# Kernel tuning notes

Measured on AMD Instinct MI355X. Metric: run time of the kernel, lower is better.

Reference implementation:

```python
import jax, jax.numpy as jnp
import numpy as np

N_NODES = 100000
N_EDGES = 1600000
N_FEAT = 128
HIDDEN = 64
NUM_GRAPHS = 64


def setup_inputs() -> dict:
    key = jax.random.key(0)
    ks = jax.random.split(key, 10)
    x = jax.random.normal(ks[0], (N_NODES, N_FEAT), dtype=jnp.float32)
    W = jax.random.normal(ks[1], (N_FEAT, HIDDEN), dtype=jnp.float32) * (1.0 / np.sqrt(N_FEAT))
    b = jax.random.normal(ks[2], (HIDDEN,), dtype=jnp.float32) * 0.01
    W1 = jax.random.normal(ks[3], (HIDDEN, 16), dtype=jnp.float32) * (1.0 / np.sqrt(HIDDEN))
    b1 = jax.random.normal(ks[4], (16,), dtype=jnp.float32) * 0.01
    W2 = jax.random.normal(ks[5], (16, 1), dtype=jnp.float32) * 0.25
    b2 = jax.random.normal(ks[6], (1,), dtype=jnp.float32) * 0.01
    edge_index = jax.random.randint(ks[7], (2, N_EDGES), 0, N_NODES, dtype=jnp.int64)
    batch = jnp.sort(jax.random.randint(ks[8], (N_NODES,), 0, NUM_GRAPHS, dtype=jnp.int64))
    return {"x": x, "W": W, "b": b, "W1": W1, "b1": b1, "W2": W2, "b2": b2,
            "edge_index": edge_index, "batch": batch, "num_graphs": NUM_GRAPHS}


def reference(x, W, b, W1, b1, W2, b2, edge_index, batch, num_graphs):
    N = x.shape[0]
    # GCNConv: h = D^-1/2 (A + I) D^-1/2 (x W) + b
    h = x @ W  # [N, H]
    loops = jnp.arange(N, dtype=edge_index.dtype)
    src = jnp.concatenate([edge_index[0], loops])  # source nodes (with self-loops)
    dst = jnp.concatenate([edge_index[1], loops])  # target nodes
    deg = jax.ops.segment_sum(jnp.ones(dst.shape, h.dtype), dst, num_segments=N)
    dis = jnp.where(deg > 0, jax.lax.rsqrt(deg), 0.0)  # deg^-1/2, 0 for isolated
    norm = dis[src] * dis[dst]  # [E+N]
    msg = h[src] * norm[:, None]  # gather + normalize
    agg = jax.ops.segment_sum(msg, dst, num_segments=N) + b  # scatter-add + bias
    hn = jax.nn.relu(agg)
    # global_add_pool over graphs
    u = jax.ops.segment_sum(hn, batch, num_segments=num_graphs)  # [G, H]
    out = jax.nn.relu(u @ W1 + b1) @ W2 + b2  # [G, 1]
    return out.reshape(-1)
```

## Files before the change

### kernel.cpp

```cpp
#include <hip/hip_runtime.h>

#define N_NODES   100000
#define N_FEAT    128
#define N_EDGES   1600000
#define HIDDEN    64
#define NUM_GRAPHS 64
#define CHUNK   8192
#define NCHUNK  ((N_EDGES + CHUNK - 1) / CHUNK)
#define BSHIFT  8
#define NBUCKET ((N_NODES + 255) >> 8)
#define OFFS_W  (NBUCKET + 1)
#define CAP     4800

typedef unsigned int  uint32;
typedef unsigned short ushort16;

typedef __attribute__((ext_vector_type(8))) __bf16 bf16x8;
typedef __attribute__((ext_vector_type(4))) float  f32x4;
union Frag8 { bf16x8 v; unsigned short s[8]; uint4 q; };

static __device__ __forceinline__ unsigned short f2bf(float f) {
    uint32 u = __float_as_uint(f);
    u += 0x7fffu + ((u >> 16) & 1u);
    return (unsigned short)(u >> 16);
}

__global__ __launch_bounds__(256) void w_transpose(const float* __restrict__ W,
                                                   ushort16* __restrict__ Wt) {
    const int base = blockIdx.x * 1024 + threadIdx.x;
#pragma unroll
    for (int j = 0; j < 4; ++j) {
        const int idx = base + j * 256;
        const int k = idx >> 6, n = idx & 63;
        Wt[n * N_FEAT + k] = f2bf(W[idx]);
    }
}

__global__ __launch_bounds__(256) void gemm_xw(const float* __restrict__ x,
                                               const ushort16* __restrict__ Wt,
                                               ushort16* __restrict__ hb) {
    const int lane = threadIdx.x & 63;
    const int wv   = threadIdx.x >> 6;
    const int m15  = lane & 15;
    const int quad = lane >> 4;
    const int base = blockIdx.x * 64 + wv * 16;
    const int arow = min(base + m15, N_NODES - 1);

    const float* xr = &x[(size_t)arow * N_FEAT + quad * 8];
    float4 xa[4][2];
#pragma unroll
    for (int kc = 0; kc < 4; ++kc) {
        xa[kc][0] = *(const float4*)&xr[kc * 32];
        xa[kc][1] = *(const float4*)&xr[kc * 32 + 4];
    }

    Frag8 bf[4][4];
#pragma unroll
    for (int nt = 0; nt < 4; ++nt) {
        const ushort16* wr = &Wt[(nt * 16 + m15) * N_FEAT + quad * 8];
#pragma unroll
        for (int kc = 0; kc < 4; ++kc)
            bf[nt][kc].q = *(const uint4*)&wr[kc * 32];
    }

    Frag8 af[4];
#pragma unroll
    for (int kc = 0; kc < 4; ++kc) {
        const float* f = (const float*)&xa[kc][0];
#pragma unroll
        for (int j = 0; j < 8; ++j) af[kc].s[j] = f2bf(f[j]);
    }

    f32x4 acc[4];
#pragma unroll
    for (int nt = 0; nt < 4; ++nt) acc[nt] = (f32x4){0.f, 0.f, 0.f, 0.f};

#pragma unroll
    for (int kc = 0; kc < 4; ++kc)
#pragma unroll
        for (int nt = 0; nt < 4; ++nt)
            acc[nt] = __builtin_amdgcn_mfma_f32_16x16x32_bf16(af[kc].v, bf[nt][kc].v,
                                                              acc[nt], 0, 0, 0);

#pragma unroll
    for (int r = 0; r < 4; ++r) {
        const int orow = base + quad * 4 + r;
        if (orow < N_NODES) {
#pragma unroll
            for (int nt = 0; nt < 4; ++nt)
                hb[(size_t)orow * HIDDEN + nt * 16 + m15] = f2bf(acc[nt][r]);
        }
    }
}

__global__ __launch_bounds__(512) void partition_kernel(const int* __restrict__ ei,
                                                        int* __restrict__ src_out,
                                                        unsigned char* __restrict__ dst8,
                                                        int* __restrict__ offs) {
    __shared__ int hist[512];
    __shared__ int excl[512];
    __shared__ int ssrc[CHUNK];
    __shared__ int sdst[CHUNK];
    const int c = blockIdx.x;
    const int base = c * CHUNK;
    const int n = min(CHUNK, N_EDGES - base);
    const int t = threadIdx.x;
    hist[t] = 0;
    __syncthreads();

    int es[CHUNK / 512], ed[CHUNK / 512], rk[CHUNK / 512];
#pragma unroll
    for (int k = 0; k < CHUNK / 512; ++k) {
        const int i = t + k * 512;
        if (i < n) {
            ed[k] = __builtin_nontemporal_load(&ei[N_EDGES + base + i]);
            es[k] = __builtin_nontemporal_load(&ei[base + i]);
            rk[k] = atomicAdd(&hist[ed[k] >> BSHIFT], 1);
        }
    }
    __syncthreads();

    const int cnt = hist[t];
    for (int off = 1; off < 512; off <<= 1) {
        const int v = (t >= off) ? hist[t - off] : 0;
        __syncthreads();
        hist[t] += v;
        __syncthreads();
    }
    excl[t] = hist[t] - cnt;
    __syncthreads();
    if (t <= NBUCKET) offs[c * OFFS_W + t] = base + excl[t];

#pragma unroll
    for (int k = 0; k < CHUNK / 512; ++k) {
        const int i = t + k * 512;
        if (i < n) {
            const int pos = excl[ed[k] >> BSHIFT] + rk[k];
            ssrc[pos] = es[k];
            sdst[pos] = ed[k];
        }
    }
    __syncthreads();

    for (int i = t; i < n; i += 512)
        src_out[base + i] = ssrc[i];
    for (int i = t * 4; i < n; i += 2048) {
        const uint32 p = (uint32)(sdst[i] & 255)
                       | ((uint32)(sdst[i + 1] & 255) << 8)
                       | ((uint32)(sdst[i + 2] & 255) << 16)
                       | ((uint32)(sdst[i + 3] & 255) << 24);
        *(uint32*)&dst8[base + i] = p;
    }
}

__global__ __launch_bounds__(512) void bucket_csr(const int* __restrict__ offs,
                                                  const int* __restrict__ src_tmp,
                                                  const unsigned char* __restrict__ dst8,
                                                  int* __restrict__ srcs,
                                                  int* __restrict__ row_ptr,
                                                  int* __restrict__ row_end,
                                                  float* __restrict__ dis) {
    __shared__ int hist[256];
    __shared__ int nxt[256];
    __shared__ int segb[NCHUNK];
    __shared__ int pre[NCHUNK + 1];
    __shared__ int sc[256];
    __shared__ int ssrc[CAP];
    __shared__ int sb;
    const int b = blockIdx.x;
    const int lo = b << BSHIFT;
    const int t = threadIdx.x;

    if (t < 256) hist[t] = 0;
    if (t == 0) sb = 0;
    __syncthreads();

    int len = 0;
    if (t < NCHUNK) {
        const int s0 = offs[t * OFFS_W + b];
        const int s1 = offs[t * OFFS_W + b + 1];
        segb[t] = s0;
        len = s1 - s0;
        atomicAdd(&sb, s0 - t * CHUNK);
    }
    if (t < 256) sc[t] = (t < NCHUNK) ? len : 0;
    __syncthreads();
    for (int off = 1; off < 256; off <<= 1) {
        int v = 0;
        if (t < 256 && t >= off) v = sc[t - off];
        __syncthreads();
        if (t < 256) sc[t] += v;
        __syncthreads();
    }
    if (t == 0) pre[0] = 0;
    if (t < NCHUNK) pre[t + 1] = sc[t];
    __syncthreads();

    const int total  = pre[NCHUNK];
    const int bstart = sb;
    const bool fits  = (total <= CAP);

    int es[(CAP + 511) / 512], ed[(CAP + 511) / 512], rk[(CAP + 511) / 512];
    int ne = 0;
    if (fits) {
        for (int e = t; e < total; e += 512) {
            int l2 = 0, h2 = NCHUNK;
            while (h2 - l2 > 1) { const int mid = (l2 + h2) >> 1;
                                  if (pre[mid] <= e) l2 = mid; else h2 = mid; }
            const int gidx = segb[l2] + (e - pre[l2]);
            const int d = dst8[gidx];
            const int s = src_tmp[gidx];
            es[ne] = s; ed[ne] = d;
            rk[ne] = atomicAdd(&hist[d], 1);
            ++ne;
        }
    } else {
        const int lane = t & 63, wv = t >> 6;
        for (int c = wv; c < NCHUNK; c += 8)
            for (int i = segb[c] + lane; i < segb[c] + (pre[c + 1] - pre[c]); i += 64)
                atomicAdd(&hist[dst8[i]], 1);
    }
    __syncthreads();

    const int cnt = (t < 256) ? hist[t] : 0;
    for (int off = 1; off < 256; off <<= 1) {
        int v = 0;
        if (t < 256 && t >= off) v = hist[t - off];
        __syncthreads();
        if (t < 256) hist[t] += v;
        __syncthreads();
    }
    if (t < 256) {
        const int excl = hist[t] - cnt;
        nxt[t] = excl;
        const int node = lo + t;
        if (node < N_NODES) {
            row_ptr[node] = bstart + excl;
            row_end[node] = bstart + excl + cnt;
            dis[node]     = rsqrtf((float)cnt + 1.0f);
        }
    }
    __syncthreads();

    if (fits) {
        for (int k = 0; k < ne; ++k)
            ssrc[nxt[ed[k]] + rk[k]] = es[k];
        __syncthreads();
        for (int i = t; i < total; i += 512)
            srcs[bstart + i] = ssrc[i];
    } else {
        const int lane = t & 63, wv = t >> 6;
        for (int c = wv; c < NCHUNK; c += 8)
            for (int i = segb[c] + lane; i < segb[c] + (pre[c + 1] - pre[c]); i += 64) {
                const int d = dst8[i];
                const int pos = atomicAdd(&nxt[d], 1);
                srcs[bstart + pos] = src_tmp[i];
            }
    }
}

__global__ __launch_bounds__(256) void agg_kernel(const int* __restrict__ row_ptr,
                                                  const int* __restrict__ row_end,
                                                  const int* __restrict__ srcs,
                                                  const ushort16* __restrict__ hb,
                                                  const float* __restrict__ dis,
                                                  const float* __restrict__ bias,
                                                  const int* __restrict__ batch,
                                                  float* __restrict__ u) {
    __shared__ float sp[32][HIDDEN + 1];
    __shared__ int gbs[32];
    const int t = threadIdx.x;
    const int lane = t & 63;
    const int wv = t >> 6;
    const int g = lane >> 3;
    const int k = lane & 7;
    const int kb = lane & 56;
    const int base = blockIdx.x * 32;
    const int node = base + wv * 8 + g;
    const int beg = row_ptr[node];
    const int end = row_end[node];
    const int deg = end - beg;
    const float dn = dis[node];

    int dmax = deg;
    dmax = max(dmax, __shfl_xor(dmax, 8));
    dmax = max(dmax, __shfl_xor(dmax, 16));
    dmax = max(dmax, __shfl_xor(dmax, 32));

    float acc[8];
#pragma unroll
    for (int j = 0; j < 8; ++j) acc[j] = 0.f;

    for (int i0 = 0; i0 < dmax; i0 += 8) {
        int idx = beg + i0 + k;
        idx = min(idx, end - 1);
        idx = max(idx, 0);
        const int s8 = srcs[idx];
        const float w8 = dis[s8] * dn;

        int   si[8];
        float wi[8];
#pragma unroll
        for (int j = 0; j < 8; ++j) {
            si[j] = __shfl(s8, kb | j);
            const float w = __shfl(w8, kb | j);
            wi[j] = (i0 + j < deg) ? w : 0.f;
        }
        uint4 v[8];
#pragma unroll
        for (int j = 0; j < 8; ++j)
            v[j] = *(const uint4*)&hb[(size_t)si[j] * HIDDEN + k * 8];
#pragma unroll
        for (int j = 0; j < 8; ++j) {
            acc[0] = fmaf(__uint_as_float(v[j].x << 16),         wi[j], acc[0]);
            acc[1] = fmaf(__uint_as_float(v[j].x & 0xffff0000u), wi[j], acc[1]);
            acc[2] = fmaf(__uint_as_float(v[j].y << 16),         wi[j], acc[2]);
            acc[3] = fmaf(__uint_as_float(v[j].y & 0xffff0000u), wi[j], acc[3]);
            acc[4] = fmaf(__uint_as_float(v[j].z << 16),         wi[j], acc[4]);
            acc[5] = fmaf(__uint_as_float(v[j].z & 0xffff0000u), wi[j], acc[5]);
            acc[6] = fmaf(__uint_as_float(v[j].w << 16),         wi[j], acc[6]);
            acc[7] = fmaf(__uint_as_float(v[j].w & 0xffff0000u), wi[j], acc[7]);
        }
    }

    {
        const uint4 hv = *(const uint4*)&hb[(size_t)node * HIDDEN + k * 8];
        const float d2 = dn * dn;
        const float4 b0 = *(const float4*)&bias[k * 8];
        const float4 b1 = *(const float4*)&bias[k * 8 + 4];
        float4 r0, r1;
        r0.x = fmaxf(fmaf(__uint_as_float(hv.x << 16),         d2, acc[0]) + b0.x, 0.f);
        r0.y = fmaxf(fmaf(__uint_as_float(hv.x & 0xffff0000u), d2, acc[1]) + b0.y, 0.f);
        r0.z = fmaxf(fmaf(__uint_as_float(hv.y << 16),         d2, acc[2]) + b0.z, 0.f);
        r0.w = fmaxf(fmaf(__uint_as_float(hv.y & 0xffff0000u), d2, acc[3]) + b0.w, 0.f);
        r1.x = fmaxf(fmaf(__uint_as_float(hv.z << 16),         d2, acc[4]) + b1.x, 0.f);
        r1.y = fmaxf(fmaf(__uint_as_float(hv.z & 0xffff0000u), d2, acc[5]) + b1.y, 0.f);
        r1.z = fmaxf(fmaf(__uint_as_float(hv.w << 16),         d2, acc[6]) + b1.z, 0.f);
        r1.w = fmaxf(fmaf(__uint_as_float(hv.w & 0xffff0000u), d2, acc[7]) + b1.w, 0.f);
        *(float4*)&sp[wv * 8 + g][k * 8]     = r0;
        *(float4*)&sp[wv * 8 + g][k * 8 + 4] = r1;
    }
    if (t < 32) gbs[t] = batch[base + t];
    __syncthreads();

    if (t < 64) {
        float a = sp[0][t];
        int cg = gbs[0];
        for (int r = 1; r < 32; ++r) {
            const int gr = gbs[r];
            const float vv = sp[r][t];
            if (gr == cg) a += vv;
            else { atomicAdd(&u[cg * HIDDEN + t], a); cg = gr; a = vv; }
        }
        atomicAdd(&u[cg * HIDDEN + t], a);
    }
}

__global__ __launch_bounds__(64) void mlp_kernel(const float* __restrict__ u,
                                                 const float* __restrict__ W1,
                                                 const float* __restrict__ b1,
                                                 const float* __restrict__ W2,
                                                 const float* __restrict__ b2,
                                                 float* __restrict__ out) {
    __shared__ float W1s[HIDDEN * 16];
    __shared__ float W2s[16];
    __shared__ float b1s[16];
    const int t = threadIdx.x;
    for (int i = t; i < HIDDEN * 16; i += 64) W1s[i] = W1[i];
    if (t < 16) { W2s[t] = W2[t]; b1s[t] = b1[t]; }
    __syncthreads();
    if (t < NUM_GRAPHS) {
        float uu[HIDDEN];
#pragma unroll
        for (int k = 0; k < HIDDEN; ++k) uu[k] = u[t * HIDDEN + k];
        float o = b2[0];
#pragma unroll
        for (int j = 0; j < 16; ++j) {
            float s = b1s[j];
#pragma unroll
            for (int k = 0; k < HIDDEN; ++k) s = fmaf(uu[k], W1s[k * 16 + j], s);
            o = fmaf(fmaxf(s, 0.f), W2s[j], o);
        }
        out[t] = o;
    }
}

extern "C" void kernel_launch(void* const* d_in, const int* in_sizes, int n_in,
                              void* d_out, int out_size, void* d_ws, size_t ws_size,
                              hipStream_t stream) {
    const float* x  = (const float*)d_in[0];
    const float* W  = (const float*)d_in[1];
    const float* b  = (const float*)d_in[2];
    const float* W1 = (const float*)d_in[3];
    const float* b1 = (const float*)d_in[4];
    const float* W2 = (const float*)d_in[5];
    const float* b2 = (const float*)d_in[6];
    const int*   ei = (const int*)d_in[7];
    const int* batch = (const int*)d_in[8];
    float* out = (float*)d_out;

    ushort16* hb       = (ushort16*)d_ws;
    int*      src_tmp  = (int*)(hb + (size_t)N_NODES * HIDDEN);
    unsigned char* dst8 = (unsigned char*)(src_tmp + N_EDGES);
    int*      srcs     = (int*)(dst8 + N_EDGES);
    int*      offs     = srcs + N_EDGES;
    int*      row_ptr  = offs + NCHUNK * OFFS_W;
    int*      row_end  = row_ptr + N_NODES;
    float*    dis      = (float*)(row_end + N_NODES);
    float*    u        = dis + N_NODES;
    ushort16* Wtg      = (ushort16*)(u + NUM_GRAPHS * HIDDEN);

    hipMemsetAsync(u, 0, NUM_GRAPHS * HIDDEN * sizeof(float), stream);

    w_transpose<<<8, 256, 0, stream>>>(W, Wtg);
    gemm_xw<<<(N_NODES + 63) / 64, 256, 0, stream>>>(x, Wtg, hb);
    partition_kernel<<<NCHUNK, 512, 0, stream>>>(ei, src_tmp, dst8, offs);
    bucket_csr<<<NBUCKET, 512, 0, stream>>>(offs, src_tmp, dst8,
                                            srcs, row_ptr, row_end, dis);
    agg_kernel<<<N_NODES / 32, 256, 0, stream>>>(row_ptr, row_end, srcs, hb, dis, b, batch, u);
    mlp_kernel<<<1, 64, 0, stream>>>(u, W1, b1, W2, b2, out);
}
```

Measured before the change: 191.0 us.

## Merge kernels into three launches with last-block MLP tail

Folds the W transpose into the partition kernel as extra blocks, runs the x·W GEMM as extra blocks of the bucket CSR kernel, and folds the final MLP into the aggregation kernel using an atomic done-counter so the last block computes the output. This cuts the launch count from six to three and lets the independent GEMM overlap the CSR build. The cost is that GEMM blocks now carry the CSR kernel's large shared memory allocation, which may lower occupancy. The aggregation kernel also pays a fence and atomic per block.

```diff
diff --git a/kernel.cpp b/kernel.cpp
--- a/kernel.cpp
+++ b/kernel.cpp
@@ -11,6 +11,8 @@
 #define NBUCKET ((N_NODES + 255) >> 8)
 #define OFFS_W  (NBUCKET + 1)
 #define CAP     4800
+#define WT_BLOCKS 4
+#define GEMM_GRID ((N_NODES + 127) / 128)
 
 typedef unsigned int  uint32;
 typedef unsigned short ushort16;
@@ -25,83 +27,29 @@
     return (unsigned short)(u >> 16);
 }
 
-__global__ __launch_bounds__(256) void w_transpose(const float* __restrict__ W,
-                                                   ushort16* __restrict__ Wt) {
-    const int base = blockIdx.x * 1024 + threadIdx.x;
-#pragma unroll
-    for (int j = 0; j < 4; ++j) {
-        const int idx = base + j * 256;
-        const int k = idx >> 6, n = idx & 63;
-        Wt[n * N_FEAT + k] = f2bf(W[idx]);
-    }
-}
-
-__global__ __launch_bounds__(256) void gemm_xw(const float* __restrict__ x,
-                                               const ushort16* __restrict__ Wt,
-                                               ushort16* __restrict__ hb) {
-    const int lane = threadIdx.x & 63;
-    const int wv   = threadIdx.x >> 6;
-    const int m15  = lane & 15;
-    const int quad = lane >> 4;
-    const int base = blockIdx.x * 64 + wv * 16;
-    const int arow = min(base + m15, N_NODES - 1);
-
-    const float* xr = &x[(size_t)arow * N_FEAT + quad * 8];
-    float4 xa[4][2];
-#pragma unroll
-    for (int kc = 0; kc < 4; ++kc) {
-        xa[kc][0] = *(const float4*)&xr[kc * 32];
-        xa[kc][1] = *(const float4*)&xr[kc * 32 + 4];
-    }
-
-    Frag8 bf[4][4];
-#pragma unroll
-    for (int nt = 0; nt < 4; ++nt) {
-        const ushort16* wr = &Wt[(nt * 16 + m15) * N_FEAT + quad * 8];
-#pragma unroll
-        for (int kc = 0; kc < 4; ++kc)
-            bf[nt][kc].q = *(const uint4*)&wr[kc * 32];
-    }
-
-    Frag8 af[4];
-#pragma unroll
-    for (int kc = 0; kc < 4; ++kc) {
-        const float* f = (const float*)&xa[kc][0];
-#pragma unroll
-        for (int j = 0; j < 8; ++j) af[kc].s[j] = f2bf(f[j]);
-    }
-
-    f32x4 acc[4];
-#pragma unroll
-    for (int nt = 0; nt < 4; ++nt) acc[nt] = (f32x4){0.f, 0.f, 0.f, 0.f};
-
-#pragma unroll
-    for (int kc = 0; kc < 4; ++kc)
-#pragma unroll
-        for (int nt = 0; nt < 4; ++nt)
-            acc[nt] = __builtin_amdgcn_mfma_f32_16x16x32_bf16(af[kc].v, bf[nt][kc].v,
-                                                              acc[nt], 0, 0, 0);
-
-#pragma unroll
-    for (int r = 0; r < 4; ++r) {
-        const int orow = base + quad * 4 + r;
-        if (orow < N_NODES) {
-#pragma unroll
-            for (int nt = 0; nt < 4; ++nt)
-                hb[(size_t)orow * HIDDEN + nt * 16 + m15] = f2bf(acc[nt][r]);
-        }
-    }
-}
-
-__global__ __launch_bounds__(512) void partition_kernel(const int* __restrict__ ei,
-                                                        int* __restrict__ src_out,
-                                                        unsigned char* __restrict__ dst8,
-                                                        int* __restrict__ offs) {
+__global__ __launch_bounds__(512) void k_pre(const float* __restrict__ W,
+                                             ushort16* __restrict__ Wt,
+                                             const int* __restrict__ ei,
+                                             int* __restrict__ src_out,
+                                             unsigned char* __restrict__ dst8,
+                                             int* __restrict__ offs) {
     __shared__ int hist[512];
     __shared__ int excl[512];
     __shared__ int ssrc[CHUNK];
     __shared__ int sdst[CHUNK];
-    const int c = blockIdx.x;
+
+    if (blockIdx.x < WT_BLOCKS) {
+        const int base = blockIdx.x * 2048 + threadIdx.x;
+#pragma unroll
+        for (int j = 0; j < 4; ++j) {
+            const int idx = base + j * 512;
+            const int k = idx >> 6, n = idx & 63;
+            Wt[n * N_FEAT + k] = f2bf(W[idx]);
+        }
+        return;
+    }
+
+    const int c = blockIdx.x - WT_BLOCKS;
     const int base = c * CHUNK;
     const int n = min(CHUNK, N_EDGES - base);
     const int t = threadIdx.x;
@@ -153,13 +101,16 @@
     }
 }
 
-__global__ __launch_bounds__(512) void bucket_csr(const int* __restrict__ offs,
-                                                  const int* __restrict__ src_tmp,
-                                                  const unsigned char* __restrict__ dst8,
-                                                  int* __restrict__ srcs,
-                                                  int* __restrict__ row_ptr,
-                                                  int* __restrict__ row_end,
-                                                  float* __restrict__ dis) {
+__global__ __launch_bounds__(512) void k_mid(const float* __restrict__ x,
+                                             const ushort16* __restrict__ Wt,
+                                             ushort16* __restrict__ hb,
+                                             const int* __restrict__ offs,
+                                             const int* __restrict__ src_tmp,
+                                             const unsigned char* __restrict__ dst8,
+                                             int* __restrict__ srcs,
+                                             int* __restrict__ row_ptr,
+                                             int* __restrict__ row_end,
+                                             float* __restrict__ dis) {
     __shared__ int hist[256];
     __shared__ int nxt[256];
     __shared__ int segb[NCHUNK];
@@ -167,6 +118,64 @@
     __shared__ int sc[256];
     __shared__ int ssrc[CAP];
     __shared__ int sb;
+
+    if (blockIdx.x >= NBUCKET) {
+        const int t    = threadIdx.x;
+        const int lane = t & 63;
+        const int wv   = t >> 6;
+        const int m15  = lane & 15;
+        const int quad = lane >> 4;
+        const int base = (blockIdx.x - NBUCKET) * 128 + wv * 16;
+        const int arow = min(base + m15, N_NODES - 1);
+
+        const float* xr = &x[(size_t)arow * N_FEAT + quad * 8];
+        float4 xa[4][2];
+#pragma unroll
+        for (int kc = 0; kc < 4; ++kc) {
+            xa[kc][0] = *(const float4*)&xr[kc * 32];
+            xa[kc][1] = *(const float4*)&xr[kc * 32 + 4];
+        }
+
+        Frag8 bf[4][4];
+#pragma unroll
+        for (int nt = 0; nt < 4; ++nt) {
+            const ushort16* wr = &Wt[(nt * 16 + m15) * N_FEAT + quad * 8];
+#pragma unroll
+            for (int kc = 0; kc < 4; ++kc)
+                bf[nt][kc].q = *(const uint4*)&wr[kc * 32];
+        }
+
+        Frag8 af[4];
+#pragma unroll
+        for (int kc = 0; kc < 4; ++kc) {
+            const float* f = (const float*)&xa[kc][0];
+#pragma unroll
+            for (int j = 0; j < 8; ++j) af[kc].s[j] = f2bf(f[j]);
+        }
+
+        f32x4 acc[4];
+#pragma unroll
+        for (int nt = 0; nt < 4; ++nt) acc[nt] = (f32x4){0.f, 0.f, 0.f, 0.f};
+
+#pragma unroll
+        for (int kc = 0; kc < 4; ++kc)
+#pragma unroll
+            for (int nt = 0; nt < 4; ++nt)
+                acc[nt] = __builtin_amdgcn_mfma_f32_16x16x32_bf16(af[kc].v, bf[nt][kc].v,
+                                                                  acc[nt], 0, 0, 0);
+
+#pragma unroll
+        for (int r = 0; r < 4; ++r) {
+            const int orow = base + quad * 4 + r;
+            if (orow < N_NODES) {
+#pragma unroll
+                for (int nt = 0; nt < 4; ++nt)
+                    hb[(size_t)orow * HIDDEN + nt * 16 + m15] = f2bf(acc[nt][r]);
+            }
+        }
+        return;
+    }
+
     const int b = blockIdx.x;
     const int lo = b << BSHIFT;
     const int t = threadIdx.x;
@@ -266,9 +275,19 @@
                                                   const float* __restrict__ dis,
                                                   const float* __restrict__ bias,
                                                   const int* __restrict__ batch,
-                                                  float* __restrict__ u) {
+                                                  float* __restrict__ u,
+                                                  const float* __restrict__ W1,
+                                                  const float* __restrict__ b1,
+                                                  const float* __restrict__ W2,
+                                                  const float* __restrict__ b2,
+                                                  float* __restrict__ out,
+                                                  int* __restrict__ done) {
     __shared__ float sp[32][HIDDEN + 1];
     __shared__ int gbs[32];
+    __shared__ int amLast;
+    __shared__ float W1s[HIDDEN * 16];
+    __shared__ float W2s[16];
+    __shared__ float b1s[16];
     const int t = threadIdx.x;
     const int lane = t & 63;
     const int wv = t >> 6;
@@ -327,16 +346,16 @@
         const uint4 hv = *(const uint4*)&hb[(size_t)node * HIDDEN + k * 8];
         const float d2 = dn * dn;
         const float4 b0 = *(const float4*)&bias[k * 8];
-        const float4 b1 = *(const float4*)&bias[k * 8 + 4];
+        const float4 b1v = *(const float4*)&bias[k * 8 + 4];
         float4 r0, r1;
         r0.x = fmaxf(fmaf(__uint_as_float(hv.x << 16),         d2, acc[0]) + b0.x, 0.f);
         r0.y = fmaxf(fmaf(__uint_as_float(hv.x & 0xffff0000u), d2, acc[1]) + b0.y, 0.f);
         r0.z = fmaxf(fmaf(__uint_as_float(hv.y << 16),         d2, acc[2]) + b0.z, 0.f);
         r0.w = fmaxf(fmaf(__uint_as_float(hv.y & 0xffff0000u), d2, acc[3]) + b0.w, 0.f);
-        r1.x = fmaxf(fmaf(__uint_as_float(hv.z << 16),         d2, acc[4]) + b1.x, 0.f);
-        r1.y = fmaxf(fmaf(__uint_as_float(hv.z & 0xffff0000u), d2, acc[5]) + b1.y, 0.f);
-        r1.z = fmaxf(fmaf(__uint_as_float(hv.w << 16),         d2, acc[6]) + b1.z, 0.f);
-        r1.w = fmaxf(fmaf(__uint_as_float(hv.w & 0xffff0000u), d2, acc[7]) + b1.w, 0.f);
+        r1.x = fmaxf(fmaf(__uint_as_float(hv.z << 16),         d2, acc[4]) + b1v.x, 0.f);
+        r1.y = fmaxf(fmaf(__uint_as_float(hv.z & 0xffff0000u), d2, acc[5]) + b1v.y, 0.f);
+        r1.z = fmaxf(fmaf(__uint_as_float(hv.w << 16),         d2, acc[6]) + b1v.z, 0.f);
+        r1.w = fmaxf(fmaf(__uint_as_float(hv.w & 0xffff0000u), d2, acc[7]) + b1v.w, 0.f);
         *(float4*)&sp[wv * 8 + g][k * 8]     = r0;
         *(float4*)&sp[wv * 8 + g][k * 8 + 4] = r1;
     }
@@ -354,31 +373,31 @@
         }
         atomicAdd(&u[cg * HIDDEN + t], a);
     }
-}
-
-__global__ __launch_bounds__(64) void mlp_kernel(const float* __restrict__ u,
-                                                 const float* __restrict__ W1,
-                                                 const float* __restrict__ b1,
-                                                 const float* __restrict__ W2,
-                                                 const float* __restrict__ b2,
-                                                 float* __restrict__ out) {
-    __shared__ float W1s[HIDDEN * 16];
-    __shared__ float W2s[16];
-    __shared__ float b1s[16];
-    const int t = threadIdx.x;
-    for (int i = t; i < HIDDEN * 16; i += 64) W1s[i] = W1[i];
+
+    __syncthreads();
+    if (t == 0) {
+        __threadfence();
+        amLast = (atomicAdd(done, 1) == (int)gridDim.x - 1) ? 1 : 0;
+    }
+    __syncthreads();
+    if (!amLast) return;
+    __threadfence();
+
+    for (int i = t; i < HIDDEN * 16; i += 256) W1s[i] = W1[i];
     if (t < 16) { W2s[t] = W2[t]; b1s[t] = b1[t]; }
     __syncthreads();
     if (t < NUM_GRAPHS) {
         float uu[HIDDEN];
 #pragma unroll
-        for (int k = 0; k < HIDDEN; ++k) uu[k] = u[t * HIDDEN + k];
+        for (int kk = 0; kk < HIDDEN; ++kk)
+            uu[kk] = __hip_atomic_load(&u[t * HIDDEN + kk], __ATOMIC_RELAXED,
+                                       __HIP_MEMORY_SCOPE_AGENT);
         float o = b2[0];
 #pragma unroll
         for (int j = 0; j < 16; ++j) {
             float s = b1s[j];
 #pragma unroll
-            for (int k = 0; k < HIDDEN; ++k) s = fmaf(uu[k], W1s[k * 16 + j], s);
+            for (int kk = 0; kk < HIDDEN; ++kk) s = fmaf(uu[kk], W1s[kk * 16 + j], s);
             o = fmaf(fmaxf(s, 0.f), W2s[j], o);
         }
         out[t] = o;
@@ -408,15 +427,14 @@
     int*      row_end  = row_ptr + N_NODES;
     float*    dis      = (float*)(row_end + N_NODES);
     float*    u        = dis + N_NODES;
-    ushort16* Wtg      = (ushort16*)(u + NUM_GRAPHS * HIDDEN);
-
-    hipMemsetAsync(u, 0, NUM_GRAPHS * HIDDEN * sizeof(float), stream);
-
-    w_transpose<<<8, 256, 0, stream>>>(W, Wtg);
-    gemm_xw<<<(N_NODES + 63) / 64, 256, 0, stream>>>(x, Wtg, hb);
-    partition_kernel<<<NCHUNK, 512, 0, stream>>>(ei, src_tmp, dst8, offs);
-    bucket_csr<<<NBUCKET, 512, 0, stream>>>(offs, src_tmp, dst8,
-                                            srcs, row_ptr, row_end, dis);
-    agg_kernel<<<N_NODES / 32, 256, 0, stream>>>(row_ptr, row_end, srcs, hb, dis, b, batch, u);
-    mlp_kernel<<<1, 64, 0, stream>>>(u, W1, b1, W2, b2, out);
+    int*      done     = (int*)(u + NUM_GRAPHS * HIDDEN);
+    ushort16* Wtg      = (ushort16*)(done + 4);
+
+    hipMemsetAsync(u, 0, NUM_GRAPHS * HIDDEN * sizeof(float) + 16, stream);
+
+    k_pre<<<WT_BLOCKS + NCHUNK, 512, 0, stream>>>(W, Wtg, ei, src_tmp, dst8, offs);
+    k_mid<<<NBUCKET + GEMM_GRID, 512, 0, stream>>>(x, Wtg, hb, offs, src_tmp, dst8,
+                                                   srcs, row_ptr, row_end, dis);
+    agg_kernel<<<N_NODES / 32, 256, 0, stream>>>(row_ptr, row_end, srcs, hb, dis, b,
+                                                 batch, u, W1, b1, W2, b2, out, done);
 }
```

Result: slower. 239.7 us (+25.5%).

## Merge independent kernels into two heterogeneous launches to cut launch count

Applied to the files above, without the earlier changes.

Merges the W transpose into the edge-partition kernel and the x@W GEMM into the bucket-CSR kernel, using blockIdx ranges to dispatch the two roles. This cuts the launch count from four to two and lets the GEMM blocks run alongside the CSR build, hiding one behind the other. In exchange, GEMM blocks now run at 512 threads with 128 rows each, and they carry the larger shared-memory footprint of the CSR kernel, which may reduce occupancy.

```diff
diff --git a/kernel.cpp b/kernel.cpp
--- a/kernel.cpp
+++ b/kernel.cpp
@@ -11,6 +11,8 @@
 #define NBUCKET ((N_NODES + 255) >> 8)
 #define OFFS_W  (NBUCKET + 1)
 #define CAP     4800
+#define WT_BLOCKS 4
+#define GEMM_GRID ((N_NODES + 127) / 128)
 
 typedef unsigned int  uint32;
 typedef unsigned short ushort16;
@@ -25,83 +27,29 @@
     return (unsigned short)(u >> 16);
 }
 
-__global__ __launch_bounds__(256) void w_transpose(const float* __restrict__ W,
-                                                   ushort16* __restrict__ Wt) {
-    const int base = blockIdx.x * 1024 + threadIdx.x;
-#pragma unroll
-    for (int j = 0; j < 4; ++j) {
-        const int idx = base + j * 256;
-        const int k = idx >> 6, n = idx & 63;
-        Wt[n * N_FEAT + k] = f2bf(W[idx]);
-    }
-}
-
-__global__ __launch_bounds__(256) void gemm_xw(const float* __restrict__ x,
-                                               const ushort16* __restrict__ Wt,
-                                               ushort16* __restrict__ hb) {
-    const int lane = threadIdx.x & 63;
-    const int wv   = threadIdx.x >> 6;
-    const int m15  = lane & 15;
-    const int quad = lane >> 4;
-    const int base = blockIdx.x * 64 + wv * 16;
-    const int arow = min(base + m15, N_NODES - 1);
-
-    const float* xr = &x[(size_t)arow * N_FEAT + quad * 8];
-    float4 xa[4][2];
-#pragma unroll
-    for (int kc = 0; kc < 4; ++kc) {
-        xa[kc][0] = *(const float4*)&xr[kc * 32];
-        xa[kc][1] = *(const float4*)&xr[kc * 32 + 4];
-    }
-
-    Frag8 bf[4][4];
-#pragma unroll
-    for (int nt = 0; nt < 4; ++nt) {
-        const ushort16* wr = &Wt[(nt * 16 + m15) * N_FEAT + quad * 8];
-#pragma unroll
-        for (int kc = 0; kc < 4; ++kc)
-            bf[nt][kc].q = *(const uint4*)&wr[kc * 32];
-    }
-
-    Frag8 af[4];
-#pragma unroll
-    for (int kc = 0; kc < 4; ++kc) {
-        const float* f = (const float*)&xa[kc][0];
-#pragma unroll
-        for (int j = 0; j < 8; ++j) af[kc].s[j] = f2bf(f[j]);
-    }
-
-    f32x4 acc[4];
-#pragma unroll
-    for (int nt = 0; nt < 4; ++nt) acc[nt] = (f32x4){0.f, 0.f, 0.f, 0.f};
-
-#pragma unroll
-    for (int kc = 0; kc < 4; ++kc)
-#pragma unroll
-        for (int nt = 0; nt < 4; ++nt)
-            acc[nt] = __builtin_amdgcn_mfma_f32_16x16x32_bf16(af[kc].v, bf[nt][kc].v,
-                                                              acc[nt], 0, 0, 0);
-
-#pragma unroll
-    for (int r = 0; r < 4; ++r) {
-        const int orow = base + quad * 4 + r;
-        if (orow < N_NODES) {
-#pragma unroll
-            for (int nt = 0; nt < 4; ++nt)
-                hb[(size_t)orow * HIDDEN + nt * 16 + m15] = f2bf(acc[nt][r]);
-        }
-    }
-}
-
-__global__ __launch_bounds__(512) void partition_kernel(const int* __restrict__ ei,
-                                                        int* __restrict__ src_out,
-                                                        unsigned char* __restrict__ dst8,
-                                                        int* __restrict__ offs) {
+__global__ __launch_bounds__(512) void k_pre(const float* __restrict__ W,
+                                             ushort16* __restrict__ Wt,
+                                             const int* __restrict__ ei,
+                                             int* __restrict__ src_out,
+                                             unsigned char* __restrict__ dst8,
+                                             int* __restrict__ offs) {
     __shared__ int hist[512];
     __shared__ int excl[512];
     __shared__ int ssrc[CHUNK];
     __shared__ int sdst[CHUNK];
-    const int c = blockIdx.x;
+
+    if (blockIdx.x < WT_BLOCKS) {
+        const int base = blockIdx.x * 2048 + threadIdx.x;
+#pragma unroll
+        for (int j = 0; j < 4; ++j) {
+            const int idx = base + j * 512;
+            const int k = idx >> 6, n = idx & 63;
+            Wt[n * N_FEAT + k] = f2bf(W[idx]);
+        }
+        return;
+    }
+
+    const int c = blockIdx.x - WT_BLOCKS;
     const int base = c * CHUNK;
     const int n = min(CHUNK, N_EDGES - base);
     const int t = threadIdx.x;
@@ -153,13 +101,16 @@
     }
 }
 
-__global__ __launch_bounds__(512) void bucket_csr(const int* __restrict__ offs,
-                                                  const int* __restrict__ src_tmp,
-                                                  const unsigned char* __restrict__ dst8,
-                                                  int* __restrict__ srcs,
-                                                  int* __restrict__ row_ptr,
-                                                  int* __restrict__ row_end,
-                                                  float* __restrict__ dis) {
+__global__ __launch_bounds__(512) void k_mid(const float* __restrict__ x,
+                                             const ushort16* __restrict__ Wt,
+                                             ushort16* __restrict__ hb,
+                                             const int* __restrict__ offs,
+                                             const int* __restrict__ src_tmp,
+                                             const unsigned char* __restrict__ dst8,
+                                             int* __restrict__ srcs,
+                                             int* __restrict__ row_ptr,
+                                             int* __restrict__ row_end,
+                                             float* __restrict__ dis) {
     __shared__ int hist[256];
     __shared__ int nxt[256];
     __shared__ int segb[NCHUNK];
@@ -167,6 +118,64 @@
     __shared__ int sc[256];
     __shared__ int ssrc[CAP];
     __shared__ int sb;
+
+    if (blockIdx.x >= NBUCKET) {
+        const int t    = threadIdx.x;
+        const int lane = t & 63;
+        const int wv   = t >> 6;
+        const int m15  = lane & 15;
+        const int quad = lane >> 4;
+        const int base = (blockIdx.x - NBUCKET) * 128 + wv * 16;
+        const int arow = min(base + m15, N_NODES - 1);
+
+        const float* xr = &x[(size_t)arow * N_FEAT + quad * 8];
+        float4 xa[4][2];
+#pragma unroll
+        for (int kc = 0; kc < 4; ++kc) {
+            xa[kc][0] = *(const float4*)&xr[kc * 32];
+            xa[kc][1] = *(const float4*)&xr[kc * 32 + 4];
+        }
+
+        Frag8 bf[4][4];
+#pragma unroll
+        for (int nt = 0; nt < 4; ++nt) {
+            const ushort16* wr = &Wt[(nt * 16 + m15) * N_FEAT + quad * 8];
+#pragma unroll
+            for (int kc = 0; kc < 4; ++kc)
+                bf[nt][kc].q = *(const uint4*)&wr[kc * 32];
+        }
+
+        Frag8 af[4];
+#pragma unroll
+        for (int kc = 0; kc < 4; ++kc) {
+            const float* f = (const float*)&xa[kc][0];
+#pragma unroll
+            for (int j = 0; j < 8; ++j) af[kc].s[j] = f2bf(f[j]);
+        }
+
+        f32x4 acc[4];
+#pragma unroll
+        for (int nt = 0; nt < 4; ++nt) acc[nt] = (f32x4){0.f, 0.f, 0.f, 0.f};
+
+#pragma unroll
+        for (int kc = 0; kc < 4; ++kc)
+#pragma unroll
+            for (int nt = 0; nt < 4; ++nt)
+                acc[nt] = __builtin_amdgcn_mfma_f32_16x16x32_bf16(af[kc].v, bf[nt][kc].v,
+                                                                  acc[nt], 0, 0, 0);
+
+#pragma unroll
+        for (int r = 0; r < 4; ++r) {
+            const int orow = base + quad * 4 + r;
+            if (orow < N_NODES) {
+#pragma unroll
+                for (int nt = 0; nt < 4; ++nt)
+                    hb[(size_t)orow * HIDDEN + nt * 16 + m15] = f2bf(acc[nt][r]);
+            }
+        }
+        return;
+    }
+
     const int b = blockIdx.x;
     const int lo = b << BSHIFT;
     const int t = threadIdx.x;
@@ -412,11 +421,9 @@
 
     hipMemsetAsync(u, 0, NUM_GRAPHS * HIDDEN * sizeof(float), stream);
 
-    w_transpose<<<8, 256, 0, stream>>>(W, Wtg);
-    gemm_xw<<<(N_NODES + 63) / 64, 256, 0, stream>>>(x, Wtg, hb);
-    partition_kernel<<<NCHUNK, 512, 0, stream>>>(ei, src_tmp, dst8, offs);
-    bucket_csr<<<NBUCKET, 512, 0, stream>>>(offs, src_tmp, dst8,
-                                            srcs, row_ptr, row_end, dis);
+    k_pre<<<WT_BLOCKS + NCHUNK, 512, 0, stream>>>(W, Wtg, ei, src_tmp, dst8, offs);
+    k_mid<<<NBUCKET + GEMM_GRID, 512, 0, stream>>>(x, Wtg, hb, offs, src_tmp, dst8,
+                                                   srcs, row_ptr, row_end, dis);
     agg_kernel<<<N_NODES / 32, 256, 0, stream>>>(row_ptr, row_end, srcs, hb, dis, b, batch, u);
     mlp_kernel<<<1, 64, 0, stream>>>(u, W1, b1, W2, b2, out);
 }
```

Result: faster. 177.4 us (-7.1%).
